# Kernel optimization log

Hardware: AMD Instinct MI355X
Metric: run time of the kernel (lower is better)

The kernel has to match this reference:

```python
import jax, jax.numpy as jnp
import numpy as np

NEG_SLOPE = 0.2


def gat_conv(x, src, dst, W, a_src, a_dst, bias, heads, out_ch, concat, num_nodes):
    # x: [N, F_in]; W: [F_in, heads*out_ch]
    h = (x @ W).reshape(num_nodes, heads, out_ch)          # [N, H, C]
    alpha_s = jnp.sum(h * a_src, axis=-1)                   # [N, H]
    alpha_d = jnp.sum(h * a_dst, axis=-1)                   # [N, H]
    e = jax.nn.leaky_relu(alpha_s[src] + alpha_d[dst], NEG_SLOPE)  # [E, H]
    # segment softmax over destination node (numerically stable)
    m = jax.ops.segment_max(e, dst, num_segments=num_nodes)        # [N, H]
    e = jnp.exp(e - m[dst])
    denom = jax.ops.segment_sum(e, dst, num_segments=num_nodes)    # [N, H]
    alpha = e / (denom[dst] + 1e-16)                               # [E, H]
    msg = h[src] * alpha[:, :, None]                               # [E, H, C]
    out = jax.ops.segment_sum(msg, dst, num_segments=num_nodes)    # [N, H, C]
    if concat:
        out = out.reshape(num_nodes, heads * out_ch)
    else:
        out = out.mean(axis=1)
    return out + bias


def setup_inputs() -> dict:
    key = jax.random.key(0)
    ks = jax.random.split(key, 12)
    N, E, F_in, H, C = 50000, 800000, 30, 4, 128
    s = lambda fan: 1.0 / np.sqrt(fan)
    inp = {
        "x": jax.random.normal(ks[0], (N, F_in), jnp.float32),
        "edge_index": jax.random.randint(ks[1], (2, E), 0, N, jnp.int32),
        "W1": jax.random.normal(ks[2], (F_in, H * C), jnp.float32) * s(F_in),
        "a1_src": jax.random.normal(ks[3], (H, C), jnp.float32) * s(C),
        "a1_dst": jax.random.normal(ks[4], (H, C), jnp.float32) * s(C),
        "b1": jnp.zeros((H * C,), jnp.float32),
        "W2": jax.random.normal(ks[5], (H * C, H * C), jnp.float32) * s(H * C),
        "a2_src": jax.random.normal(ks[6], (H, C), jnp.float32) * s(C),
        "a2_dst": jax.random.normal(ks[7], (H, C), jnp.float32) * s(C),
        "b2": jnp.zeros((H * C,), jnp.float32),
        "W3": jax.random.normal(ks[8], (H * C, H * 1), jnp.float32) * s(H * C),
        "a3_src": jax.random.normal(ks[9], (H, 1), jnp.float32),
        "a3_dst": jax.random.normal(ks[10], (H, 1), jnp.float32),
        "b3": jnp.zeros((1,), jnp.float32),
    }
    return inp


def reference(x, edge_index, W1, a1_src, a1_dst, b1, W2, a2_src, a2_dst, b2,
              W3, a3_src, a3_dst, b3):
    N = x.shape[0]
    # PyG GATConv adds self loops by default
    loop = jnp.arange(N, dtype=edge_index.dtype)
    src = jnp.concatenate([edge_index[0], loop])
    dst = jnp.concatenate([edge_index[1], loop])

    h = gat_conv(x, src, dst, W1, a1_src, a1_dst, b1, 4, 128, True, N)
    h = jax.nn.relu(h)  # dropout is a no-op in eval mode
    h = gat_conv(h, src, dst, W2, a2_src, a2_dst, b2, 4, 128, True, N)
    h = jax.nn.relu(h)
    out = gat_conv(h, src, dst, W3, a3_src, a3_dst, b3, 4, 1, False, N)
    return out  # [N, 1]
```

## Files before the change

kernel.cpp:

```cpp
#include <hip/hip_runtime.h>

#define NEG_SLOPE 0.2f

constexpr int F = 512;
constexpr int F_IN = 30;
constexpr int DMAX = 512;

typedef short bfrag __attribute__((ext_vector_type(8)));
typedef float f32x4 __attribute__((ext_vector_type(4)));

__device__ __forceinline__ unsigned short bf16_rne(float v) {
  unsigned u = __float_as_uint(v);
  u += 0x7FFF + ((u >> 16) & 1);
  return (unsigned short)(u >> 16);
}
__device__ __forceinline__ float bf16f(unsigned short h) {
  return __uint_as_float(((unsigned)h) << 16);
}


__global__ void hist_kernel(const int* __restrict__ ei, int* __restrict__ counts,
                            int N, int E) {
  int e = blockIdx.x * blockDim.x + threadIdx.x;
  int Et = E + N;
  if (e >= Et) return;
  int d = (e < E) ? ei[E + e] : (e - E);
  atomicAdd(&counts[d], 1);
}

__global__ void blockscan_kernel(const int* __restrict__ counts, int* __restrict__ offsets,
                                 int* __restrict__ bsums, int n) {
  __shared__ int wsum[16];
  int tid = threadIdx.x;
  int lane = tid & 63, wid = tid >> 6;
  int i = blockIdx.x * 1024 + tid;
  int v = (i < n) ? counts[i] : 0;
  int x = v;
#pragma unroll
  for (int d = 1; d < 64; d <<= 1) {
    int t2 = __shfl_up(x, d);
    if (lane >= d) x += t2;
  }
  if (lane == 63) wsum[wid] = x;
  __syncthreads();
  if (wid == 0) {
    int ws = (lane < 16) ? wsum[lane] : 0;
#pragma unroll
    for (int d = 1; d < 16; d <<= 1) {
      int t2 = __shfl_up(ws, d);
      if (lane >= d) ws += t2;
    }
    if (lane < 16) wsum[lane] = ws;
  }
  __syncthreads();
  int excl = ((wid > 0) ? wsum[wid - 1] : 0) + x - v;
  if (i < n) offsets[i] = excl;
  if (tid == 0) bsums[blockIdx.x] = wsum[15];
}

__global__ void sumscan_kernel(const int* __restrict__ bsums, int* __restrict__ boffs, int nb) {
  __shared__ int wsum[16];
  int tid = threadIdx.x;
  int lane = tid & 63, wid = tid >> 6;
  int v = (tid < nb) ? bsums[tid] : 0;
  int x = v;
#pragma unroll
  for (int d = 1; d < 64; d <<= 1) {
    int t2 = __shfl_up(x, d);
    if (lane >= d) x += t2;
  }
  if (lane == 63) wsum[wid] = x;
  __syncthreads();
  if (wid == 0) {
    int ws = (lane < 16) ? wsum[lane] : 0;
#pragma unroll
    for (int d = 1; d < 16; d <<= 1) {
      int t2 = __shfl_up(ws, d);
      if (lane >= d) ws += t2;
    }
    if (lane < 16) wsum[lane] = ws;
  }
  __syncthreads();
  int excl = ((wid > 0) ? wsum[wid - 1] : 0) + x - v;
  if (tid <= nb) boffs[tid] = (tid < nb) ? excl : wsum[15];
  if (tid == 0 && nb == 1024) boffs[1024] = wsum[15];
}

__global__ void scanadd_kernel(int* __restrict__ offsets, const int* __restrict__ boffs,
                               int* __restrict__ cursor, int n, int nb) {
  int i = blockIdx.x * blockDim.x + threadIdx.x;
  if (i < n) {
    int o = offsets[i] + boffs[i >> 10];
    offsets[i] = o;
    cursor[i] = o;
  } else if (i == n) {
    offsets[n] = boffs[nb];
  }
}

__global__ void scatter_kernel(const int* __restrict__ ei, int* __restrict__ cursor,
                               int* __restrict__ src_s, int N, int E) {
  int e = blockIdx.x * blockDim.x + threadIdx.x;
  int Et = E + N;
  if (e >= Et) return;
  int s, d;
  if (e < E) { s = ei[e]; d = ei[E + e]; } else { s = e - E; d = e - E; }
  int p = atomicAdd(&cursor[d], 1);
  src_s[p] = s;
}

__global__ void segsort_kernel(int* __restrict__ src_s, const int* __restrict__ off, int N) {
  __shared__ int buf[128][65];
  int n = blockIdx.x * 128 + threadIdx.x;
  if (n >= N) return;
  int p0 = off[n], p1 = off[n + 1];
  int deg = p1 - p0;
  if (deg <= 64) {
    int* b = buf[threadIdx.x];
    for (int i = 0; i < deg; ++i) b[i] = src_s[p0 + i];
    for (int i = 1; i < deg; ++i) {
      int key = b[i];
      int j = i - 1;
      while (j >= 0 && b[j] > key) { b[j + 1] = b[j]; --j; }
      b[j + 1] = key;
    }
    for (int i = 0; i < deg; ++i) src_s[p0 + i] = b[i];
  } else {
    for (int i = p0 + 1; i < p1; ++i) {
      int key = src_s[i];
      int j = i - 1;
      while (j >= p0 && src_s[j] > key) { src_s[j + 1] = src_s[j]; --j; }
      src_s[j + 1] = key;
    }
  }
}


__global__ void gemm30_kernel(const float* __restrict__ X, const float* __restrict__ W,
                              const float* __restrict__ a_s, const float* __restrict__ a_d,
                              float* __restrict__ out,
                              float* __restrict__ as_o, float* __restrict__ ad_o, int N) {
  __shared__ float xs[16][F_IN];
  int row0 = blockIdx.x * 16;
  int tid = threadIdx.x;
  for (int i = tid; i < 16 * F_IN; i += 256) {
    int r = i / F_IN, k = i - r * F_IN;
    int row = row0 + r;
    xs[r][k] = (row < N) ? X[(size_t)row * F_IN + k] : 0.f;
  }
  __syncthreads();
  int cg = tid & 127;
  int rg = tid >> 7;
  int c0 = cg * 4;
  float4 acc[8];
#pragma unroll
  for (int r = 0; r < 8; ++r) acc[r] = make_float4(0.f, 0.f, 0.f, 0.f);
#pragma unroll 2
  for (int k = 0; k < F_IN; ++k) {
    float4 w = *(const float4*)(W + (size_t)k * F + c0);
#pragma unroll
    for (int r = 0; r < 8; ++r) {
      float xv = xs[rg * 8 + r][k];
      acc[r].x += xv * w.x; acc[r].y += xv * w.y;
      acc[r].z += xv * w.z; acc[r].w += xv * w.w;
    }
  }
#pragma unroll
  for (int r = 0; r < 8; ++r) {
    int row = row0 + rg * 8 + r;
    if (row < N) *(float4*)(out + (size_t)row * F + c0) = acc[r];
  }
  int hd = cg >> 5;
  float4 s4 = *(const float4*)(a_s + c0);
  float4 d4 = *(const float4*)(a_d + c0);
#pragma unroll
  for (int r = 0; r < 8; ++r) {
    float ps = acc[r].x * s4.x + acc[r].y * s4.y + acc[r].z * s4.z + acc[r].w * s4.w;
    float pd = acc[r].x * d4.x + acc[r].y * d4.y + acc[r].z * d4.z + acc[r].w * d4.w;
#pragma unroll
    for (int o = 1; o < 32; o <<= 1) {
      ps += __shfl_xor(ps, o, 32);
      pd += __shfl_xor(pd, o, 32);
    }
    if ((tid & 31) == 0) {
      int row = row0 + rg * 8 + r;
      if (row < N) { as_o[row * 4 + hd] = ps; ad_o[row * 4 + hd] = pd; }
    }
  }
}


__global__ void wsplit_kernel(const float* __restrict__ W,
                              unsigned short* __restrict__ Wth,
                              unsigned short* __restrict__ Wtl) {
  __shared__ float t[64][65];
  int bx = blockIdx.x & 7, by = blockIdx.x >> 3;
  int tid = threadIdx.x;
#pragma unroll
  for (int i = 0; i < 16; ++i) {
    int idx = tid + i * 256;
    int r = idx >> 6, c = idx & 63;
    t[r][c] = W[(size_t)(by * 64 + r) * 512 + bx * 64 + c];
  }
  __syncthreads();
#pragma unroll
  for (int i = 0; i < 16; ++i) {
    int idx = tid + i * 256;
    int r = idx >> 6, c = idx & 63;
    float v = t[c][r];
    unsigned short hi = bf16_rne(v);
    unsigned short lo = bf16_rne(v - bf16f(hi));
    size_t o = (size_t)(bx * 64 + r) * 512 + by * 64 + c;
    Wth[o] = hi; Wtl[o] = lo;
  }
}


__global__ void gemm512_mfma(const unsigned short* __restrict__ Xhi,
                             const unsigned short* __restrict__ Xlo,
                             const unsigned short* __restrict__ Wth,
                             const unsigned short* __restrict__ Wtl,
                             const float* __restrict__ a_s, const float* __restrict__ a_d,
                             float* __restrict__ out,
                             float* __restrict__ as_o, float* __restrict__ ad_o, int N) {
  __shared__ int4 lds4[2048];
  char* lds = (char*)lds4;
  const int tid = threadIdx.x;
  const int wid = tid >> 6;
  const int lane = tid & 63;
  const int row0 = blockIdx.x * 128;
  const int by = blockIdx.y;
  const int col0 = by * 128;
  const int wr = wid >> 1, wc = wid & 1;

  const unsigned short* sb = (wid == 0) ? Xhi : (wid == 1) ? Xlo : (wid == 2) ? Wth : Wtl;
  const int tile0 = (wid < 2) ? row0 : col0;
  const int chunk = (lane & 3) ^ ((lane >> 3) & 3);
  const unsigned short* lanesrc = sb + (size_t)(tile0 + (lane >> 2)) * 512 + chunk * 8;
  char* ldst = lds + wid * 8192;

  const int g = lane >> 4;
  int aoff[4], boff[4];
#pragma unroll
  for (int m = 0; m < 4; ++m) {
    int r = wr * 64 + m * 16 + (lane & 15);
    aoff[m] = r * 64 + ((g ^ ((r >> 1) & 3)) << 4);
    int c = wc * 64 + m * 16 + (lane & 15);
    boff[m] = c * 64 + ((g ^ ((c >> 1) & 3)) << 4);
  }

  f32x4 acc[4][4];
#pragma unroll
  for (int m = 0; m < 4; ++m)
#pragma unroll
    for (int n = 0; n < 4; ++n) acc[m][n] = f32x4{0.f, 0.f, 0.f, 0.f};

  for (int kc = 0; kc < 16; ++kc) {
#pragma unroll
    for (int i = 0; i < 8; ++i) {
      __builtin_amdgcn_global_load_lds(
          (const __attribute__((address_space(1))) void*)(lanesrc + i * 8192 + kc * 32),
          (__attribute__((address_space(3))) void*)(ldst + i * 1024), 16, 0, 0);
    }
    __syncthreads();
    bfrag ah[4], al[4], bh[4], bl[4];
#pragma unroll
    for (int m = 0; m < 4; ++m) {
      ah[m] = *(const bfrag*)(lds + aoff[m]);
      al[m] = *(const bfrag*)(lds + 8192 + aoff[m]);
      bh[m] = *(const bfrag*)(lds + 16384 + boff[m]);
      bl[m] = *(const bfrag*)(lds + 24576 + boff[m]);
    }
#pragma unroll
    for (int m = 0; m < 4; ++m)
#pragma unroll
      for (int n = 0; n < 4; ++n) {
        acc[m][n] = __builtin_amdgcn_mfma_f32_16x16x32_bf16(al[m], bh[n], acc[m][n], 0, 0, 0);
        acc[m][n] = __builtin_amdgcn_mfma_f32_16x16x32_bf16(ah[m], bl[n], acc[m][n], 0, 0, 0);
        acc[m][n] = __builtin_amdgcn_mfma_f32_16x16x32_bf16(ah[m], bh[n], acc[m][n], 0, 0, 0);
      }
    __syncthreads();
  }

  const int crow = (lane >> 4) * 4, ccol = lane & 15;
#pragma unroll
  for (int m = 0; m < 4; ++m) {
    int Rb = row0 + wr * 64 + m * 16 + crow;
#pragma unroll
    for (int n = 0; n < 4; ++n) {
      int C = col0 + wc * 64 + n * 16 + ccol;
#pragma unroll
      for (int q = 0; q < 4; ++q) {
        int R = Rb + q;
        if (R < N) out[(size_t)R * F + C] = acc[m][n][q];
      }
    }
  }

  float cs[4], cd[4];
#pragma unroll
  for (int n = 0; n < 4; ++n) {
    cs[n] = a_s[col0 + wc * 64 + n * 16 + (lane & 15)];
    cd[n] = a_d[col0 + wc * 64 + n * 16 + (lane & 15)];
  }
  float* red = (float*)lds;
#pragma unroll
  for (int m = 0; m < 4; ++m) {
#pragma unroll
    for (int q = 0; q < 4; ++q) {
      float ps = 0.f, pd = 0.f;
#pragma unroll
      for (int n = 0; n < 4; ++n) {
        ps += acc[m][n][q] * cs[n];
        pd += acc[m][n][q] * cd[n];
      }
#pragma unroll
      for (int o = 1; o < 16; o <<= 1) {
        ps += __shfl_xor(ps, o, 16);
        pd += __shfl_xor(pd, o, 16);
      }
      if ((lane & 15) == 0) {
        int rl = m * 16 + (lane >> 4) * 4 + q;
        red[((wr * 2 + wc) * 64 + rl) * 2 + 0] = ps;
        red[((wr * 2 + wc) * 64 + rl) * 2 + 1] = pd;
      }
    }
  }
  __syncthreads();
  if (tid < 128) {
    int wrr = tid >> 6, rl = tid & 63;
    float vs = red[((wrr * 2 + 0) * 64 + rl) * 2] + red[((wrr * 2 + 1) * 64 + rl) * 2];
    float vd = red[((wrr * 2 + 0) * 64 + rl) * 2 + 1] + red[((wrr * 2 + 1) * 64 + rl) * 2 + 1];
    int row = row0 + wrr * 64 + rl;
    if (row < N) { as_o[row * 4 + by] = vs; ad_o[row * 4 + by] = vd; }
  }
}


__device__ __forceinline__ float leaky(float v) { return v > 0.f ? v : NEG_SLOPE * v; }

__device__ __forceinline__ void fma4(float4& a, float s, const float4& b) {
  a.x += s * b.x; a.y += s * b.y; a.z += s * b.z; a.w += s * b.w;
}

template <bool RELU, bool SPLIT, bool H3>
__global__ void fused_aggregate_kernel(const float* __restrict__ hsrc,
                                       const float* __restrict__ as, const float* __restrict__ ad,
                                       const int* __restrict__ src_s, const int* __restrict__ off,
                                       const float* __restrict__ bias, float* __restrict__ out,
                                       unsigned short* __restrict__ oh, unsigned short* __restrict__ ol,
                                       const float* __restrict__ W3, const float* __restrict__ a3s,
                                       const float* __restrict__ a3d, float* __restrict__ h3_o,
                                       float* __restrict__ as3_o, float* __restrict__ ad3_o) {
  __shared__ float esc[4][DMAX + 8];
  __shared__ float hred[2][4];
  int n = blockIdx.x;
  int tid = threadIdx.x;
  int head = tid >> 5;
  int l32 = tid & 31;
  int c0 = tid * 4;
  int p0 = off[n], p1 = off[n + 1];
  int deg = p1 - p0;
  float4 adv4 = *(const float4*)(ad + (size_t)n * 4);
  float adv = (head == 0) ? adv4.x : (head == 1) ? adv4.y : (head == 2) ? adv4.z : adv4.w;

  float m = -1e30f, s = 0.f;
  float4 acc = make_float4(0.f, 0.f, 0.f, 0.f);

  if (deg <= DMAX) {
    for (int i = tid; i < deg; i += 128) {
      int sp = src_s[p0 + i];
      float4 a4 = *(const float4*)(as + (size_t)sp * 4);
      esc[0][i] = leaky(a4.x + adv4.x);
      esc[1][i] = leaky(a4.y + adv4.y);
      esc[2][i] = leaky(a4.z + adv4.z);
      esc[3][i] = leaky(a4.w + adv4.w);
    }
    __syncthreads();
    for (int i = l32; i < deg; i += 32) {
      float e = esc[head][i];
      if (e > m) { s *= __expf(m - e); m = e; }
      s += __expf(e - m);
    }
#pragma unroll
    for (int o = 16; o > 0; o >>= 1) {
      float mo = __shfl_down(m, o, 32);
      float so = __shfl_down(s, o, 32);
      float mn = fmaxf(m, mo);
      s = s * __expf(m - mn) + so * __expf(mo - mn);
      m = mn;
    }
    m = __shfl(m, 0, 32);
    s = __shfl(s, 0, 32);
    float inv = 1.f / (s + 1e-16f);
#pragma unroll 2
    for (int i = 0; i < deg; ++i) {
      int sp = src_s[p0 + i];
      float a = __expf(esc[head][i] - m) * inv;
      float4 hv = *(const float4*)(hsrc + (size_t)sp * F + c0);
      fma4(acc, a, hv);
    }
  } else {
    for (int p = p0 + l32; p < p1; p += 32) {
      float e = leaky(as[src_s[p] * 4 + head] + adv);
      if (e > m) { s *= __expf(m - e); m = e; }
      s += __expf(e - m);
    }
#pragma unroll
    for (int o = 16; o > 0; o >>= 1) {
      float mo = __shfl_down(m, o, 32);
      float so = __shfl_down(s, o, 32);
      float mn = fmaxf(m, mo);
      s = s * __expf(m - mn) + so * __expf(mo - mn);
      m = mn;
    }
    m = __shfl(m, 0, 32);
    s = __shfl(s, 0, 32);
    float inv = 1.f / (s + 1e-16f);
    for (int p = p0; p < p1; ++p) {
      int sp = src_s[p];
      float a = __expf(leaky(as[sp * 4 + head] + adv) - m) * inv;
      float4 hv = *(const float4*)(hsrc + (size_t)sp * F + c0);
      fma4(acc, a, hv);
    }
  }

  float4 bv = *(const float4*)(bias + c0);
  acc.x += bv.x; acc.y += bv.y; acc.z += bv.z; acc.w += bv.w;
  if (RELU) {
    acc.x = fmaxf(acc.x, 0.f); acc.y = fmaxf(acc.y, 0.f);
    acc.z = fmaxf(acc.z, 0.f); acc.w = fmaxf(acc.w, 0.f);
  }
  if (SPLIT) {
    ushort4 hv4, lv4;
    hv4.x = bf16_rne(acc.x); lv4.x = bf16_rne(acc.x - bf16f(hv4.x));
    hv4.y = bf16_rne(acc.y); lv4.y = bf16_rne(acc.y - bf16f(hv4.y));
    hv4.z = bf16_rne(acc.z); lv4.z = bf16_rne(acc.z - bf16f(hv4.z));
    hv4.w = bf16_rne(acc.w); lv4.w = bf16_rne(acc.w - bf16f(hv4.w));
    *(ushort4*)(oh + (size_t)n * F + c0) = hv4;
    *(ushort4*)(ol + (size_t)n * F + c0) = lv4;
  } else if (!H3) {
    *(float4*)(out + (size_t)n * F + c0) = acc;
  }
  if (H3) {
    float4 w0 = *(const float4*)(W3 + (size_t)(c0 + 0) * 4);
    float4 w1 = *(const float4*)(W3 + (size_t)(c0 + 1) * 4);
    float4 w2 = *(const float4*)(W3 + (size_t)(c0 + 2) * 4);
    float4 w3r = *(const float4*)(W3 + (size_t)(c0 + 3) * 4);
    float p[4];
    p[0] = acc.x * w0.x + acc.y * w1.x + acc.z * w2.x + acc.w * w3r.x;
    p[1] = acc.x * w0.y + acc.y * w1.y + acc.z * w2.y + acc.w * w3r.y;
    p[2] = acc.x * w0.z + acc.y * w1.z + acc.z * w2.z + acc.w * w3r.z;
    p[3] = acc.x * w0.w + acc.y * w1.w + acc.z * w2.w + acc.w * w3r.w;
#pragma unroll
    for (int j = 0; j < 4; ++j)
#pragma unroll
      for (int o = 1; o < 64; o <<= 1) p[j] += __shfl_xor(p[j], o, 64);
    int wv = tid >> 6;
    if ((tid & 63) == 0) {
      hred[wv][0] = p[0]; hred[wv][1] = p[1];
      hred[wv][2] = p[2]; hred[wv][3] = p[3];
    }
    __syncthreads();
    if (tid == 0) {
      float4 h;
      h.x = hred[0][0] + hred[1][0];
      h.y = hred[0][1] + hred[1][1];
      h.z = hred[0][2] + hred[1][2];
      h.w = hred[0][3] + hred[1][3];
      *(float4*)(h3_o + (size_t)n * 4) = h;
      float4 so, dd;
      so.x = h.x * a3s[0]; so.y = h.y * a3s[1]; so.z = h.z * a3s[2]; so.w = h.w * a3s[3];
      dd.x = h.x * a3d[0]; dd.y = h.y * a3d[1]; dd.z = h.z * a3d[2]; dd.w = h.w * a3d[3];
      *(float4*)(as3_o + (size_t)n * 4) = so;
      *(float4*)(ad3_o + (size_t)n * 4) = dd;
    }
  }
}

__global__ void fused_aggregate3_kernel(const float* __restrict__ h3,
                                        const float* __restrict__ as, const float* __restrict__ ad,
                                        const int* __restrict__ src_s, const int* __restrict__ off,
                                        const float* __restrict__ b3, float* __restrict__ out, int N) {
  int t = blockIdx.x * blockDim.x + threadIdx.x;
  if (t >= N * 4) return;
  int n = t >> 2, head = t & 3;
  int p0 = off[n], p1 = off[n + 1];
  float adv = ad[t];
  float m = -1e30f, s = 0.f;
  for (int p = p0; p < p1; ++p) {
    float e = leaky(as[src_s[p] * 4 + head] + adv);
    if (e > m) { s *= __expf(m - e); m = e; }
    s += __expf(e - m);
  }
  float inv = 1.f / (s + 1e-16f);
  float acc = 0.f;
  for (int p = p0; p < p1; ++p) {
    int sp = src_s[p];
    float a = __expf(leaky(as[sp * 4 + head] + adv) - m) * inv;
    acc += a * h3[(size_t)sp * 4 + head];
  }
  acc += __shfl_down(acc, 1);
  acc += __shfl_down(acc, 2);
  if (head == 0) out[n] = acc * 0.25f + b3[0];
}


extern "C" void kernel_launch(void* const* d_in, const int* in_sizes, int n_in,
                              void* d_out, int out_size, void* d_ws, size_t ws_size,
                              hipStream_t stream) {
  const float* x   = (const float*)d_in[0];
  const int*   ei  = (const int*)d_in[1];
  const float* W1  = (const float*)d_in[2];
  const float* a1s = (const float*)d_in[3];
  const float* a1d = (const float*)d_in[4];
  const float* b1  = (const float*)d_in[5];
  const float* W2  = (const float*)d_in[6];
  const float* a2s = (const float*)d_in[7];
  const float* a2d = (const float*)d_in[8];
  const float* b2  = (const float*)d_in[9];
  const float* W3  = (const float*)d_in[10];
  const float* a3s = (const float*)d_in[11];
  const float* a3d = (const float*)d_in[12];
  const float* b3  = (const float*)d_in[13];

  const int N = in_sizes[0] / F_IN;
  const int E = in_sizes[1] / 2;
  const int Et = E + N;
  const int Npad = (N + 127) & ~127;
  const int nb = (N + 1023) >> 10;

  char* base = (char*)d_ws;
  size_t off = 0;
  auto alloc = [&](size_t bytes) {
    void* p = base + off;
    off = (off + bytes + 255) & ~(size_t)255;
    return p;
  };
  float* A      = (float*)alloc((size_t)N * F * sizeof(float));
  float* U      = (float*)alloc((size_t)Npad * F * sizeof(float));
  unsigned short* Xhi = (unsigned short*)U;
  unsigned short* Xlo = Xhi + (size_t)Npad * F;
  int*   src_s  = (int*)alloc((size_t)Et * sizeof(int));
  int*   counts = (int*)alloc((size_t)N * sizeof(int));
  int*   offs   = (int*)alloc((size_t)(N + 1) * sizeof(int));
  int*   cursor = (int*)alloc((size_t)N * sizeof(int));
  int*   bsums  = (int*)alloc((size_t)1025 * sizeof(int));
  int*   boffs  = (int*)alloc((size_t)1026 * sizeof(int));
  float* as     = (float*)alloc((size_t)N * 4 * sizeof(float));
  float* ad     = (float*)alloc((size_t)N * 4 * sizeof(float));
  float* as3    = (float*)alloc((size_t)N * 4 * sizeof(float));
  float* ad3    = (float*)alloc((size_t)N * 4 * sizeof(float));
  float* h3     = (float*)alloc((size_t)N * 4 * sizeof(float));
  unsigned short* Wth = (unsigned short*)alloc((size_t)512 * 512 * sizeof(unsigned short));
  unsigned short* Wtl = (unsigned short*)alloc((size_t)512 * 512 * sizeof(unsigned short));

  hipMemsetAsync(counts, 0, (size_t)N * sizeof(int), stream);
  {
    int gg = (Et + 255) / 256;
    hipLaunchKernelGGL(hist_kernel, dim3(gg), dim3(256), 0, stream, ei, counts, N, E);
    hipLaunchKernelGGL(blockscan_kernel, dim3(nb), dim3(1024), 0, stream, counts, offs, bsums, N);
    hipLaunchKernelGGL(sumscan_kernel, dim3(1), dim3(1024), 0, stream, bsums, boffs, nb);
    hipLaunchKernelGGL(scanadd_kernel, dim3((N + 256) / 256), dim3(256), 0, stream, offs, boffs, cursor, N, nb);
    hipLaunchKernelGGL(scatter_kernel, dim3(gg), dim3(256), 0, stream, ei, cursor, src_s, N, E);
    hipLaunchKernelGGL(segsort_kernel, dim3((N + 127) / 128), dim3(128), 0, stream, src_s, offs, N);
    hipLaunchKernelGGL(wsplit_kernel, dim3(64), dim3(256), 0, stream, W2, Wth, Wtl);
  }

  int nhGrid = (N * 4 + 255) / 256;

  hipLaunchKernelGGL(gemm30_kernel, dim3((N + 15) / 16), dim3(256), 0, stream,
                     x, W1, a1s, a1d, A, as, ad, N);
  hipLaunchKernelGGL((fused_aggregate_kernel<true, true, false>), dim3(N), dim3(128), 0, stream,
                     A, as, ad, src_s, offs, b1, (float*)nullptr, Xhi, Xlo,
                     (const float*)nullptr, (const float*)nullptr, (const float*)nullptr,
                     (float*)nullptr, (float*)nullptr, (float*)nullptr);

  hipLaunchKernelGGL(gemm512_mfma, dim3((N + 127) / 128, 4), dim3(256), 0, stream,
                     Xhi, Xlo, Wth, Wtl, a2s, a2d, A, as, ad, N);
  hipLaunchKernelGGL((fused_aggregate_kernel<true, false, true>), dim3(N), dim3(128), 0, stream,
                     A, as, ad, src_s, offs, b2, (float*)nullptr,
                     (unsigned short*)nullptr, (unsigned short*)nullptr,
                     W3, a3s, a3d, h3, as3, ad3);

  hipLaunchKernelGGL(fused_aggregate3_kernel, dim3(nhGrid), dim3(256), 0, stream,
                     h3, as3, ad3, src_s, offs, b3, (float*)d_out, N);
}
```

Before: 828.7 us.

## Merge independent setup kernels and parallelize final-layer aggregation across lanes

The histogram pass is folded into the first-layer GEMM launch as extra blocks, and the W2 bf16 split is folded into the scatter launch the same way. This cuts the number of launches and lets independent work share the GPU. The third-layer aggregation now gives each node a 64-lane wavefront, with 16 lanes per head. It uses an online-softmax shuffle reduction instead of one serial thread per (node, head). The cost is more shuffle and exp work and a different summation order.

```diff
diff --git a/kernel.cpp b/kernel.cpp
--- a/kernel.cpp
+++ b/kernel.cpp
@@ -18,15 +18,6 @@
   return __uint_as_float(((unsigned)h) << 16);
 }
 
-
-__global__ void hist_kernel(const int* __restrict__ ei, int* __restrict__ counts,
-                            int N, int E) {
-  int e = blockIdx.x * blockDim.x + threadIdx.x;
-  int Et = E + N;
-  if (e >= Et) return;
-  int d = (e < E) ? ei[E + e] : (e - E);
-  atomicAdd(&counts[d], 1);
-}
 
 __global__ void blockscan_kernel(const int* __restrict__ counts, int* __restrict__ offsets,
                                  int* __restrict__ bsums, int n) {
@@ -98,15 +89,42 @@
   }
 }
 
-__global__ void scatter_kernel(const int* __restrict__ ei, int* __restrict__ cursor,
-                               int* __restrict__ src_s, int N, int E) {
-  int e = blockIdx.x * blockDim.x + threadIdx.x;
-  int Et = E + N;
-  if (e >= Et) return;
-  int s, d;
-  if (e < E) { s = ei[e]; d = ei[E + e]; } else { s = e - E; d = e - E; }
-  int p = atomicAdd(&cursor[d], 1);
-  src_s[p] = s;
+__global__ void scatter_wsplit_kernel(const int* __restrict__ ei, int* __restrict__ cursor,
+                                      int* __restrict__ src_s, int N, int E, int scatGrid,
+                                      const float* __restrict__ W,
+                                      unsigned short* __restrict__ Wth,
+                                      unsigned short* __restrict__ Wtl) {
+  __shared__ float t[64][65];
+  if (blockIdx.x < scatGrid) {
+    int e = blockIdx.x * 256 + threadIdx.x;
+    int Et = E + N;
+    if (e >= Et) return;
+    int s, d;
+    if (e < E) { s = ei[e]; d = ei[E + e]; } else { s = e - E; d = e - E; }
+    int p = atomicAdd(&cursor[d], 1);
+    src_s[p] = s;
+    return;
+  }
+  int b = blockIdx.x - scatGrid;
+  int bx = b & 7, by = b >> 3;
+  int tid = threadIdx.x;
+#pragma unroll
+  for (int i = 0; i < 16; ++i) {
+    int idx = tid + i * 256;
+    int r = idx >> 6, c = idx & 63;
+    t[r][c] = W[(size_t)(by * 64 + r) * 512 + bx * 64 + c];
+  }
+  __syncthreads();
+#pragma unroll
+  for (int i = 0; i < 16; ++i) {
+    int idx = tid + i * 256;
+    int r = idx >> 6, c = idx & 63;
+    float v = t[c][r];
+    unsigned short hi = bf16_rne(v);
+    unsigned short lo = bf16_rne(v - bf16f(hi));
+    size_t o = (size_t)(bx * 64 + r) * 512 + by * 64 + c;
+    Wth[o] = hi; Wtl[o] = lo;
+  }
 }
 
 __global__ void segsort_kernel(int* __restrict__ src_s, const int* __restrict__ off, int N) {
@@ -136,13 +154,24 @@
 }
 
 
-__global__ void gemm30_kernel(const float* __restrict__ X, const float* __restrict__ W,
-                              const float* __restrict__ a_s, const float* __restrict__ a_d,
-                              float* __restrict__ out,
-                              float* __restrict__ as_o, float* __restrict__ ad_o, int N) {
+__global__ void gemm30_hist_kernel(const float* __restrict__ X, const float* __restrict__ W,
+                                   const float* __restrict__ a_s, const float* __restrict__ a_d,
+                                   float* __restrict__ out,
+                                   float* __restrict__ as_o, float* __restrict__ ad_o, int N,
+                                   const int* __restrict__ ei, int* __restrict__ counts,
+                                   int E, int gemmGrid) {
   __shared__ float xs[16][F_IN];
+  int tid = threadIdx.x;
+  if (blockIdx.x >= gemmGrid) {
+    int e = (blockIdx.x - gemmGrid) * 256 + tid;
+    int Et = E + N;
+    if (e < Et) {
+      int d = (e < E) ? ei[E + e] : (e - E);
+      atomicAdd(&counts[d], 1);
+    }
+    return;
+  }
   int row0 = blockIdx.x * 16;
-  int tid = threadIdx.x;
   for (int i = tid; i < 16 * F_IN; i += 256) {
     int r = i / F_IN, k = i - r * F_IN;
     int row = row0 + r;
@@ -186,32 +215,6 @@
       int row = row0 + rg * 8 + r;
       if (row < N) { as_o[row * 4 + hd] = ps; ad_o[row * 4 + hd] = pd; }
     }
-  }
-}
-
-
-__global__ void wsplit_kernel(const float* __restrict__ W,
-                              unsigned short* __restrict__ Wth,
-                              unsigned short* __restrict__ Wtl) {
-  __shared__ float t[64][65];
-  int bx = blockIdx.x & 7, by = blockIdx.x >> 3;
-  int tid = threadIdx.x;
-#pragma unroll
-  for (int i = 0; i < 16; ++i) {
-    int idx = tid + i * 256;
-    int r = idx >> 6, c = idx & 63;
-    t[r][c] = W[(size_t)(by * 64 + r) * 512 + bx * 64 + c];
-  }
-  __syncthreads();
-#pragma unroll
-  for (int i = 0; i < 16; ++i) {
-    int idx = tid + i * 256;
-    int r = idx >> 6, c = idx & 63;
-    float v = t[c][r];
-    unsigned short hi = bf16_rne(v);
-    unsigned short lo = bf16_rne(v - bf16f(hi));
-    size_t o = (size_t)(bx * 64 + r) * 512 + by * 64 + c;
-    Wth[o] = hi; Wtl[o] = lo;
   }
 }
 
@@ -482,27 +485,44 @@
                                         const float* __restrict__ as, const float* __restrict__ ad,
                                         const int* __restrict__ src_s, const int* __restrict__ off,
                                         const float* __restrict__ b3, float* __restrict__ out, int N) {
-  int t = blockIdx.x * blockDim.x + threadIdx.x;
-  if (t >= N * 4) return;
-  int n = t >> 2, head = t & 3;
+  int tid = threadIdx.x;
+  int n = blockIdx.x * 4 + (tid >> 6);
+  if (n >= N) return;
+  int l64 = tid & 63;
+  int head = l64 >> 4;
+  int l16 = l64 & 15;
   int p0 = off[n], p1 = off[n + 1];
-  float adv = ad[t];
+  float adv = ad[n * 4 + head];
   float m = -1e30f, s = 0.f;
-  for (int p = p0; p < p1; ++p) {
+  for (int p = p0 + l16; p < p1; p += 16) {
     float e = leaky(as[src_s[p] * 4 + head] + adv);
     if (e > m) { s *= __expf(m - e); m = e; }
     s += __expf(e - m);
   }
+#pragma unroll
+  for (int o = 8; o > 0; o >>= 1) {
+    float mo = __shfl_down(m, o, 16);
+    float so = __shfl_down(s, o, 16);
+    float mn = fmaxf(m, mo);
+    s = s * __expf(m - mn) + so * __expf(mo - mn);
+    m = mn;
+  }
+  m = __shfl(m, 0, 16);
+  s = __shfl(s, 0, 16);
   float inv = 1.f / (s + 1e-16f);
   float acc = 0.f;
-  for (int p = p0; p < p1; ++p) {
+  for (int p = p0 + l16; p < p1; p += 16) {
     int sp = src_s[p];
     float a = __expf(leaky(as[sp * 4 + head] + adv) - m) * inv;
     acc += a * h3[(size_t)sp * 4 + head];
   }
-  acc += __shfl_down(acc, 1);
-  acc += __shfl_down(acc, 2);
-  if (head == 0) out[n] = acc * 0.25f + b3[0];
+#pragma unroll
+  for (int o = 8; o > 0; o >>= 1) acc += __shfl_down(acc, o, 16);
+  float v0 = __shfl(acc, 0, 64);
+  float v1 = __shfl(acc, 16, 64);
+  float v2 = __shfl(acc, 32, 64);
+  float v3 = __shfl(acc, 48, 64);
+  if (l64 == 0) out[n] = ((v0 + v1) + (v2 + v3)) * 0.25f + b3[0];
 }
 
 
@@ -555,22 +575,20 @@
   unsigned short* Wth = (unsigned short*)alloc((size_t)512 * 512 * sizeof(unsigned short));
   unsigned short* Wtl = (unsigned short*)alloc((size_t)512 * 512 * sizeof(unsigned short));
 
+  const int gemmGrid = (N + 15) / 16;
+  const int histGrid = (Et + 255) / 256;
+  const int scatGrid = histGrid;
+
   hipMemsetAsync(counts, 0, (size_t)N * sizeof(int), stream);
-  {
-    int gg = (Et + 255) / 256;
-    hipLaunchKernelGGL(hist_kernel, dim3(gg), dim3(256), 0, stream, ei, counts, N, E);
-    hipLaunchKernelGGL(blockscan_kernel, dim3(nb), dim3(1024), 0, stream, counts, offs, bsums, N);
-    hipLaunchKernelGGL(sumscan_kernel, dim3(1), dim3(1024), 0, stream, bsums, boffs, nb);
-    hipLaunchKernelGGL(scanadd_kernel, dim3((N + 256) / 256), dim3(256), 0, stream, offs, boffs, cursor, N, nb);
-    hipLaunchKernelGGL(scatter_kernel, dim3(gg), dim3(256), 0, stream, ei, cursor, src_s, N, E);
-    hipLaunchKernelGGL(segsort_kernel, dim3((N + 127) / 128), dim3(128), 0, stream, src_s, offs, N);
-    hipLaunchKernelGGL(wsplit_kernel, dim3(64), dim3(256), 0, stream, W2, Wth, Wtl);
-  }
-
-  int nhGrid = (N * 4 + 255) / 256;
-
-  hipLaunchKernelGGL(gemm30_kernel, dim3((N + 15) / 16), dim3(256), 0, stream,
-                     x, W1, a1s, a1d, A, as, ad, N);
+  hipLaunchKernelGGL(gemm30_hist_kernel, dim3(gemmGrid + histGrid), dim3(256), 0, stream,
+                     x, W1, a1s, a1d, A, as, ad, N, ei, counts, E, gemmGrid);
+  hipLaunchKernelGGL(blockscan_kernel, dim3(nb), dim3(1024), 0, stream, counts, offs, bsums, N);
+  hipLaunchKernelGGL(sumscan_kernel, dim3(1), dim3(1024), 0, stream, bsums, boffs, nb);
+  hipLaunchKernelGGL(scanadd_kernel, dim3((N + 256) / 256), dim3(256), 0, stream, offs, boffs, cursor, N, nb);
+  hipLaunchKernelGGL(scatter_wsplit_kernel, dim3(scatGrid + 64), dim3(256), 0, stream,
+                     ei, cursor, src_s, N, E, scatGrid, W2, Wth, Wtl);
+  hipLaunchKernelGGL(segsort_kernel, dim3((N + 127) / 128), dim3(128), 0, stream, src_s, offs, N);
+
   hipLaunchKernelGGL((fused_aggregate_kernel<true, true, false>), dim3(N), dim3(128), 0, stream,
                      A, as, ad, src_s, offs, b1, (float*)nullptr, Xhi, Xlo,
                      (const float*)nullptr, (const float*)nullptr, (const float*)nullptr,
@@ -583,6 +601,6 @@
                      (unsigned short*)nullptr, (unsigned short*)nullptr,
                      W3, a3s, a3d, h3, as3, ad3);
 
-  hipLaunchKernelGGL(fused_aggregate3_kernel, dim3(nhGrid), dim3(256), 0, stream,
+  hipLaunchKernelGGL(fused_aggregate3_kernel, dim3((N + 3) / 4), dim3(256), 0, stream,
                      h3, as3, ad3, src_s, offs, b3, (float*)d_out, N);
 }
```

New measurement: 814.3 us. No clear change (-1.7%).
